# Kernel optimization log

Measured on AMD Instinct MI355X. Metric: run time of the kernel, lower is better.

Reference implementation:

```python
import jax, jax.numpy as jnp
import numpy as np

B, S, D, H = 4, 1024, 1024, 16
DK = D // H  # 64


def setup_inputs() -> dict:
    key = jax.random.key(0)
    ks = jax.random.split(key, 12)
    scale = 0.02
    inp = {
        "query": jax.random.normal(ks[0], (B, S, D), jnp.float32),
        "key": jax.random.normal(ks[1], (B, S, D), jnp.float32),
        "value": jax.random.normal(ks[2], (B, S, D), jnp.float32),
        "mask": jax.random.randint(ks[3], (B, 1, S, S), 0, 2, jnp.int32),
        "wq": jax.random.normal(ks[4], (D, D), jnp.float32) * scale,
        "bq": jnp.zeros((D,), jnp.float32),
        "wk": jax.random.normal(ks[5], (D, D), jnp.float32) * scale,
        "bk": jnp.zeros((D,), jnp.float32),
        "wv": jax.random.normal(ks[6], (D, D), jnp.float32) * scale,
        "bv": jnp.zeros((D,), jnp.float32),
        "wo": jax.random.normal(ks[7], (D, D), jnp.float32) * scale,
        "bo": jnp.zeros((D,), jnp.float32),
    }
    return inp


def reference(query, key, value, mask, wq, bq, wk, bk, wv, bv, wo, bo):
    # Linear projections (torch Linear: x @ W.T + b)
    q = query @ wq.T + bq
    k = key @ wk.T + bk
    v = value @ wv.T + bv
    # [B,S,D] -> [B,H,S,DK]
    q = q.reshape(B, S, H, DK).transpose(0, 2, 1, 3)
    k = k.reshape(B, S, H, DK).transpose(0, 2, 1, 3)
    v = v.reshape(B, S, H, DK).transpose(0, 2, 1, 3)
    # scaled dot-product attention with mask (-1e9 where mask==0)
    scores = jnp.einsum('bhqd,bhkd->bhqk', q, k) / jnp.sqrt(jnp.float32(DK))
    scores = jnp.where(mask == 0, jnp.float32(-1e9), scores)
    attn = jax.nn.softmax(scores, axis=-1)  # dropout p=0.0 -> identity
    x = jnp.einsum('bhqk,bhkd->bhqd', attn, v)
    # [B,H,S,DK] -> [B,S,D]
    x = x.transpose(0, 2, 1, 3).reshape(B, S, D)
    return x @ wo.T + bo
```

## Files before the change

kernel.cpp:

```cpp
#include <hip/hip_runtime.h>


typedef __attribute__((ext_vector_type(8))) short short8;
typedef __attribute__((ext_vector_type(4))) float f32x4;
typedef __attribute__((ext_vector_type(4))) unsigned short u16x4;
typedef unsigned short u16;
typedef unsigned long long u64;

#define SCALE_Q 0.180336880f

__device__ __forceinline__ u16 f2bf(float f) {
    unsigned u = __float_as_uint(f);
    return (u16)((u + 0x7FFFu + ((u >> 16) & 1u)) >> 16);
}
__device__ __forceinline__ u16 f2bf_fast(float f) {
    return (u16)((__float_as_uint(f) + 0x8000u) >> 16);
}
__device__ __forceinline__ float bf2f(u16 v) {
    return __uint_as_float((unsigned)v << 16);
}

__device__ __forceinline__ void gl_lds16(const u16* g, u16* l) {
    __builtin_amdgcn_global_load_lds(
        (__attribute__((address_space(1))) void*)g,
        (__attribute__((address_space(3))) void*)l, 16, 0, 0);
}

__global__ __launch_bounds__(256) void prep(
    const float* __restrict__ q, const float* __restrict__ k,
    const float* __restrict__ v, const float* __restrict__ wq,
    const float* __restrict__ wk, const float* __restrict__ wv,
    const float* __restrict__ wo, const int* __restrict__ mask,
    u16* __restrict__ xq, u16* __restrict__ xk, u16* __restrict__ xv,
    u16* __restrict__ wqb, u16* __restrict__ wkb, u16* __restrict__ wvb,
    u16* __restrict__ wob, u64* __restrict__ bits) {
    int bid = blockIdx.x;
    if (bid < 16384) {
        const float* src; u16* dst; int i;
        if (bid < 12288) {
            int chunk = bid >> 12;
            int off = bid & 4095;
            src = (chunk == 0) ? q : ((chunk == 1) ? k : v);
            dst = (chunk == 0) ? xq : ((chunk == 1) ? xk : xv);
            i = off * 256 + threadIdx.x;
        } else {
            int wb = bid - 12288;
            int chunk = wb >> 10;
            int off = wb & 1023;
            src = (chunk == 0) ? wq : ((chunk == 1) ? wk : ((chunk == 2) ? wv : wo));
            dst = (chunk == 0) ? wqb : ((chunk == 1) ? wkb : ((chunk == 2) ? wvb : wob));
            i = off * 256 + threadIdx.x;
        }
        f32x4 val = ((const f32x4*)src)[i];
        u16x4 r;
        r.x = f2bf(val.x); r.y = f2bf(val.y); r.z = f2bf(val.z); r.w = f2bf(val.w);
        ((u16x4*)dst)[i] = r;
    } else {
        int mb = bid - 16384;
        int wid = threadIdx.x >> 6, lane = threadIdx.x & 63;
        int base = mb * 1024 + wid * 256;
        int b = mb >> 10, qrow = mb & 1023;
        #pragma unroll
        for (int j = 0; j < 4; ++j) {
            u64 bal = __ballot(mask[base + j * 64 + lane] != 0);
            int kt = wid * 4 + j;
            if (lane == 0) bits[(size_t)(b * 16 + kt) * 1024 + qrow] = bal;
        }
    }
}

__global__ __launch_bounds__(256, 3) void gemm_qkv(
    const u16* __restrict__ Aq, const u16* __restrict__ Ak, const u16* __restrict__ Av,
    const u16* __restrict__ Wq, const u16* __restrict__ Wk, const u16* __restrict__ Wv,
    const float* __restrict__ bq, const float* __restrict__ bk, const float* __restrict__ bv,
    u16* __restrict__ Qo, u16* __restrict__ Ko, u16* __restrict__ VTo) {
    __shared__ __align__(16) u16 As[128 * 64];
    __shared__ __align__(16) u16 Bs[128 * 64];
    const int id = blockIdx.x;
    const int n0 = (id / 96) * 128;
    const int pm = id % 96;
    const int p = pm >> 5;
    const int m0 = (pm & 31) * 128;
    const u16* A = (p == 0) ? Aq : ((p == 1) ? Ak : Av);
    const u16* W = (p == 0) ? Wq : ((p == 1) ? Wk : Wv);
    const float* bias = (p == 0) ? bq : ((p == 1) ? bk : bv);

    const int t = threadIdx.x;
    const int lane = t & 63;
    const int wid = t >> 6;
    const int l15 = lane & 15;
    const int quad = lane >> 4;
    const int wm = (wid & 1) * 64;
    const int wn = (wid >> 1) * 64;
    const int r8 = lane >> 3, gr = lane & 7;
    const int gsw = (gr ^ r8) * 8;

    f32x4 acc[4][4];
    #pragma unroll
    for (int i = 0; i < 4; ++i)
        #pragma unroll
        for (int j = 0; j < 4; ++j) acc[i][j] = (f32x4){0.f, 0.f, 0.f, 0.f};

    for (int kt = 0; kt < 1024; kt += 64) {
        __syncthreads();
        #pragma unroll
        for (int c = 0; c < 8; ++c) {
            int call = wid * 8 + c;
            if (call < 16) {
                int rb = call * 8;
                gl_lds16(&A[(size_t)(m0 + rb + r8) * 1024 + kt + gsw], &As[rb * 64]);
            } else {
                int rb = (call - 16) * 8;
                gl_lds16(&W[(size_t)(n0 + rb + r8) * 1024 + kt + gsw], &Bs[rb * 64]);
            }
        }
        __syncthreads();
        #pragma unroll
        for (int ks = 0; ks < 2; ++ks) {
            short8 af[4], bf[4];
            #pragma unroll
            for (int i = 0; i < 4; ++i) {
                int mr = wm + i * 16 + l15;
                af[i] = *(const short8*)&As[mr * 64 + (((ks << 2) + quad) ^ (mr & 7)) * 8];
                int nr = wn + i * 16 + l15;
                bf[i] = *(const short8*)&Bs[nr * 64 + (((ks << 2) + quad) ^ (nr & 7)) * 8];
            }
            #pragma unroll
            for (int mi = 0; mi < 4; ++mi)
                #pragma unroll
                for (int ni = 0; ni < 4; ++ni)
                    acc[mi][ni] = __builtin_amdgcn_mfma_f32_16x16x32_bf16(
                        af[mi], bf[ni], acc[mi][ni], 0, 0, 0);
        }
    }

    u16* dst01 = (p == 0) ? Qo : Ko;
    const float qs = (p == 0) ? SCALE_Q : 1.0f;
    #pragma unroll
    for (int mi = 0; mi < 4; ++mi) {
        #pragma unroll
        for (int ni = 0; ni < 4; ++ni) {
            int col = n0 + wn + ni * 16 + l15;
            int h = col >> 6, dk = col & 63;
            float bcol = bias[col];
            if (p < 2) {
                #pragma unroll
                for (int r = 0; r < 4; ++r) {
                    int row = m0 + wm + mi * 16 + quad * 4 + r;
                    int bb = row >> 10, s = row & 1023;
                    dst01[(size_t)((bb * 16 + h) * 1024 + s) * 64 + dk] =
                        f2bf((acc[mi][ni][r] + bcol) * qs);
                }
            } else {
                int row0 = m0 + wm + mi * 16 + quad * 4;
                int bb = row0 >> 10, s0 = row0 & 1023;
                u64 pk = 0;
                #pragma unroll
                for (int r = 0; r < 4; ++r)
                    pk |= (u64)f2bf(acc[mi][ni][r] + bcol) << (16 * r);
                *(u64*)&VTo[(size_t)((bb * 16 + h) * 64 + dk) * 1024 + s0] = pk;
            }
        }
    }
}

__global__ __launch_bounds__(256, 3) void gemm_out(
    const u16* __restrict__ X, const u16* __restrict__ Wo,
    const float* __restrict__ bo, float* __restrict__ out) {
    __shared__ __align__(16) u16 As[64 * 64];
    __shared__ __align__(16) u16 Bs[128 * 64];
    const int id = blockIdx.x;
    const int n0 = (id >> 6) * 128;
    const int m0 = (id & 63) * 64;
    const int t = threadIdx.x;
    const int lane = t & 63;
    const int wid = t >> 6;
    const int l15 = lane & 15;
    const int quad = lane >> 4;
    const int wm = (wid & 1) * 32;
    const int wn = (wid >> 1) * 64;
    const int r8 = lane >> 3, gr = lane & 7;
    const int gsw = (gr ^ r8) * 8;

    f32x4 acc[2][4];
    #pragma unroll
    for (int i = 0; i < 2; ++i)
        #pragma unroll
        for (int j = 0; j < 4; ++j) acc[i][j] = (f32x4){0.f, 0.f, 0.f, 0.f};

    for (int kt = 0; kt < 1024; kt += 64) {
        __syncthreads();
        #pragma unroll
        for (int c = 0; c < 6; ++c) {
            int call = wid * 6 + c;
            if (call < 8) {
                int rb = call * 8;
                gl_lds16(&X[(size_t)(m0 + rb + r8) * 1024 + kt + gsw], &As[rb * 64]);
            } else {
                int rb = (call - 8) * 8;
                gl_lds16(&Wo[(size_t)(n0 + rb + r8) * 1024 + kt + gsw], &Bs[rb * 64]);
            }
        }
        __syncthreads();
        #pragma unroll
        for (int ks = 0; ks < 2; ++ks) {
            short8 af[2], bf[4];
            #pragma unroll
            for (int i = 0; i < 2; ++i) {
                int mr = wm + i * 16 + l15;
                af[i] = *(const short8*)&As[mr * 64 + (((ks << 2) + quad) ^ (mr & 7)) * 8];
            }
            #pragma unroll
            for (int j = 0; j < 4; ++j) {
                int nr = wn + j * 16 + l15;
                bf[j] = *(const short8*)&Bs[nr * 64 + (((ks << 2) + quad) ^ (nr & 7)) * 8];
            }
            #pragma unroll
            for (int mi = 0; mi < 2; ++mi)
                #pragma unroll
                for (int ni = 0; ni < 4; ++ni)
                    acc[mi][ni] = __builtin_amdgcn_mfma_f32_16x16x32_bf16(
                        af[mi], bf[ni], acc[mi][ni], 0, 0, 0);
        }
    }

    #pragma unroll
    for (int mi = 0; mi < 2; ++mi) {
        #pragma unroll
        for (int ni = 0; ni < 4; ++ni) {
            int col = n0 + wn + ni * 16 + l15;
            float bcol = bo[col];
            #pragma unroll
            for (int r = 0; r < 4; ++r) {
                int row = m0 + wm + mi * 16 + quad * 4 + r;
                out[(size_t)row * 1024 + col] = acc[mi][ni][r] + bcol;
            }
        }
    }
}

__global__ __launch_bounds__(256) void attn_kernel(
    const u16* __restrict__ Q, const u16* __restrict__ K, const u16* __restrict__ VT,
    const u64* __restrict__ mbits, u16* __restrict__ O, float* __restrict__ L) {
    __shared__ __align__(16) u16 Ks[64 * 64];
    __shared__ __align__(16) u16 Vs[64 * 64];
    __shared__ __align__(16) u16 Ps[4][16 * 72];

    const int qt = blockIdx.x;
    const int h = blockIdx.y;
    const int b = blockIdx.z >> 1;
    const int half = blockIdx.z & 1;
    const int t = threadIdx.x;
    const int lane = t & 63;
    const int wid = t >> 6;
    const int l15 = lane & 15;
    const int quad = lane >> 4;
    const int q0 = qt * 64;
    const int sr = t >> 3;
    const int sc = t & 7;
    const int ktg0 = half * 8;

    const size_t headoff = (size_t)(b * 16 + h) * 1024 * 64;
    const u16* Qh = Q + headoff;
    const u16* Kh = K + headoff;
    const u16* Vh = VT + headoff;

    short8 qf[2];
    #pragma unroll
    for (int ks = 0; ks < 2; ++ks)
        qf[ks] = *(const short8*)&Qh[(size_t)(q0 + wid * 16 + l15) * 64 + ks * 32 + quad * 8];

    f32x4 o_acc[4];
    #pragma unroll
    for (int j = 0; j < 4; ++j) o_acc[j] = (f32x4){0.f, 0.f, 0.f, 0.f};
    float lacc = 0.f;

    const u64* mbase = &mbits[(size_t)(b * 16) * 1024 + q0 + wid * 16 + l15];

    short8 kpre[2], vpre[2];
    #pragma unroll
    for (int p = 0; p < 2; ++p) {
        int r = p * 32 + sr;
        kpre[p] = *(const short8*)&Kh[(size_t)(ktg0 * 64 + r) * 64 + sc * 8];
        vpre[p] = *(const short8*)&Vh[(size_t)r * 1024 + ktg0 * 64 + sc * 8];
    }

    for (int kt = 0; kt < 8; ++kt) {
        __syncthreads();
        #pragma unroll
        for (int p = 0; p < 2; ++p) {
            int r = p * 32 + sr;
            int gl = sc ^ (r & 7);
            *(short8*)&Ks[r * 64 + gl * 8] = kpre[p];
            *(short8*)&Vs[r * 64 + gl * 8] = vpre[p];
        }
        __syncthreads();

        if (kt < 7) {
            int kvn = (ktg0 + kt + 1) * 64;
            #pragma unroll
            for (int p = 0; p < 2; ++p) {
                int r = p * 32 + sr;
                kpre[p] = *(const short8*)&Kh[(size_t)(kvn + r) * 64 + sc * 8];
                vpre[p] = *(const short8*)&Vh[(size_t)r * 1024 + kvn + sc * 8];
            }
        }

        f32x4 sacc[4];
        #pragma unroll
        for (int j = 0; j < 4; ++j) sacc[j] = (f32x4){0.f, 0.f, 0.f, 0.f};
        #pragma unroll
        for (int ks = 0; ks < 2; ++ks) {
            #pragma unroll
            for (int mi = 0; mi < 4; ++mi) {
                int n = mi * 16 + l15;
                short8 kf = *(const short8*)&Ks[n * 64 + (((ks << 2) + quad) ^ (n & 7)) * 8];
                sacc[mi] = __builtin_amdgcn_mfma_f32_16x16x32_bf16(kf, qf[ks], sacc[mi], 0, 0, 0);
            }
        }

        u64 w = mbase[(size_t)(ktg0 + kt) * 1024];
        unsigned t0 = (unsigned)(w >> (quad * 4));
        unsigned t1 = (unsigned)(w >> (quad * 4 + 32));
        #pragma unroll
        for (int mi = 0; mi < 4; ++mi) {
            unsigned sel = (mi & 2) ? t1 : t0;
            sel >>= (mi & 1) * 16;
            u64 pk = 0;
            #pragma unroll
            for (int r = 0; r < 4; ++r) {
                float p = __builtin_amdgcn_exp2f(sacc[mi][r]);
                p = ((sel >> r) & 1u) ? p : 0.f;
                lacc += p;
                pk |= (u64)f2bf_fast(p) << (16 * r);
            }
            *(u64*)&Ps[wid][l15 * 72 + mi * 16 + quad * 4] = pk;
        }

        #pragma unroll
        for (int ks = 0; ks < 2; ++ks) {
            short8 pf = *(const short8*)&Ps[wid][l15 * 72 + ks * 32 + quad * 8];
            #pragma unroll
            for (int j = 0; j < 4; ++j) {
                int d = j * 16 + l15;
                short8 vf = *(const short8*)&Vs[d * 64 + (((ks << 2) + quad) ^ (d & 7)) * 8];
                o_acc[j] = __builtin_amdgcn_mfma_f32_16x16x32_bf16(pf, vf, o_acc[j], 0, 0, 0);
            }
        }
    }

    float l = lacc;
    l += __shfl_xor(l, 16);
    l += __shfl_xor(l, 32);
    u16* Oh = O + (size_t)half * 4194304;
    float* Lh = L + (size_t)half * 65536;
    if (lane < 16)
        Lh[(size_t)(b * 16 + h) * 1024 + q0 + wid * 16 + lane] = l;
    #pragma unroll
    for (int r = 0; r < 4; ++r) {
        int qrow = q0 + wid * 16 + quad * 4 + r;
        #pragma unroll
        for (int ni = 0; ni < 4; ++ni) {
            Oh[(size_t)(b * 1024 + qrow) * 1024 + h * 64 + ni * 16 + l15] =
                f2bf(o_acc[ni][r]);
        }
    }
}

__global__ __launch_bounds__(256) void merge_halves(
    const u16* __restrict__ O, const float* __restrict__ L, u16* __restrict__ X) {
    int i = (blockIdx.x * 256 + threadIdx.x) * 8;
    int b = i >> 20, s = (i >> 10) & 1023, c = i & 1023, h = c >> 6;
    short8 o0 = *(const short8*)&O[i];
    short8 o1 = *(const short8*)&O[4194304 + i];
    size_t li = (size_t)(b * 16 + h) * 1024 + s;
    float inv = 1.0f / (L[li] + L[65536 + li]);
    short8 r;
    #pragma unroll
    for (int j = 0; j < 8; ++j) {
        float x = (bf2f((u16)o0[j]) + bf2f((u16)o1[j])) * inv;
        r[j] = (short)f2bf(x);
    }
    *(short8*)&X[i] = r;
}

extern "C" void kernel_launch(void* const* d_in, const int* in_sizes, int n_in,
                              void* d_out, int out_size, void* d_ws, size_t ws_size,
                              hipStream_t stream) {
    const float* query = (const float*)d_in[0];
    const float* key_ = (const float*)d_in[1];
    const float* value = (const float*)d_in[2];
    const int* mask = (const int*)d_in[3];
    const float* wq = (const float*)d_in[4];
    const float* bq = (const float*)d_in[5];
    const float* wk = (const float*)d_in[6];
    const float* bk = (const float*)d_in[7];
    const float* wv = (const float*)d_in[8];
    const float* bv = (const float*)d_in[9];
    const float* wo = (const float*)d_in[10];
    const float* bo = (const float*)d_in[11];
    float* out = (float*)d_out;

    char* ws = (char*)d_ws;
    const size_t XB = (size_t)4096 * 1024 * 2;
    const size_t WB = (size_t)1024 * 1024 * 2;
    u16* xq = (u16*)(ws);
    u16* xk = (u16*)(ws + XB);
    u16* xv = (u16*)(ws + 2 * XB);
    u16* wqb = (u16*)(ws + 3 * XB);
    u16* wkb = (u16*)(ws + 3 * XB + WB);
    u16* wvb = (u16*)(ws + 3 * XB + 2 * WB);
    u16* wob = (u16*)(ws + 3 * XB + 3 * WB);
    u16* Qb = (u16*)(ws + 3 * XB + 4 * WB);
    u16* Kb = (u16*)(ws + 4 * XB + 4 * WB);
    u16* VTb = (u16*)(ws + 5 * XB + 4 * WB);
    u64* bits = (u64*)(ws + 6 * XB + 4 * WB);
    float* Lbuf = (float*)(ws + 6 * XB + 4 * WB + (512 << 10));
    u16* Opart = xk;
    u16* Xattn = xq;

    prep<<<20480, 256, 0, stream>>>(query, key_, value, wq, wk, wv, wo, mask,
                                    xq, xk, xv, wqb, wkb, wvb, wob, bits);
    gemm_qkv<<<768, 256, 0, stream>>>(xq, xk, xv, wqb, wkb, wvb,
                                      bq, bk, bv, Qb, Kb, VTb);
    attn_kernel<<<dim3(16, 16, 8), 256, 0, stream>>>(Qb, Kb, VTb, bits, Opart, Lbuf);
    merge_halves<<<2048, 256, 0, stream>>>(Opart, Lbuf, Xattn);
    gemm_out<<<512, 256, 0, stream>>>(Xattn, wob, bo, out);
}
```

Baseline: 222.2 us.

## Fuse split-KV merge into output GEMM and double query rows per attention block

Removes the merge_halves kernel by performing the two-half normalization and bf16 conversion inside gemm_out's A-tile load, writing the merged tile into LDS directly instead of via async global-to-LDS copies. The attention kernel now processes 32 query rows per wave (128 per block), reusing each K/V LDS tile across twice as many queries and halving the grid. This cuts a kernel launch and a full intermediate write/read, but the merge math is recomputed by each of the 8 N-column blocks sharing an M tile. The attention kernel also uses more registers per thread.

```diff
diff --git a/kernel.cpp b/kernel.cpp
--- a/kernel.cpp
+++ b/kernel.cpp
@@ -165,8 +165,9 @@
 }
 
 __global__ __launch_bounds__(256, 3) void gemm_out(
-    const u16* __restrict__ X, const u16* __restrict__ Wo,
-    const float* __restrict__ bo, float* __restrict__ out) {
+    const u16* __restrict__ O, const float* __restrict__ L,
+    const u16* __restrict__ Wo, const float* __restrict__ bo,
+    float* __restrict__ out) {
     __shared__ __align__(16) u16 As[64 * 64];
     __shared__ __align__(16) u16 Bs[128 * 64];
     const int id = blockIdx.x;
@@ -181,6 +182,7 @@
     const int wn = (wid >> 1) * 64;
     const int r8 = lane >> 3, gr = lane & 7;
     const int gsw = (gr ^ r8) * 8;
+    const int sr = t >> 3, sc = t & 7;
 
     f32x4 acc[2][4];
     #pragma unroll
@@ -189,17 +191,28 @@
         for (int j = 0; j < 4; ++j) acc[i][j] = (f32x4){0.f, 0.f, 0.f, 0.f};
 
     for (int kt = 0; kt < 1024; kt += 64) {
-        __syncthreads();
-        #pragma unroll
-        for (int c = 0; c < 6; ++c) {
-            int call = wid * 6 + c;
-            if (call < 8) {
-                int rb = call * 8;
-                gl_lds16(&X[(size_t)(m0 + rb + r8) * 1024 + kt + gsw], &As[rb * 64]);
-            } else {
-                int rb = (call - 8) * 8;
-                gl_lds16(&Wo[(size_t)(n0 + rb + r8) * 1024 + kt + gsw], &Bs[rb * 64]);
-            }
+        const int h = kt >> 6;
+        __syncthreads();
+        #pragma unroll
+        for (int p = 0; p < 2; ++p) {
+            int r = p * 32 + sr;
+            int row = m0 + r;
+            int b = row >> 10, s = row & 1023;
+            size_t li = (size_t)((b * 16 + h) << 10) + s;
+            float inv = 1.0f / (L[li] + L[65536 + li]);
+            size_t go = (size_t)row * 1024 + kt + sc * 8;
+            short8 o0 = *(const short8*)&O[go];
+            short8 o1 = *(const short8*)&O[4194304 + go];
+            short8 xm;
+            #pragma unroll
+            for (int j = 0; j < 8; ++j)
+                xm[j] = (short)f2bf((bf2f((u16)o0[j]) + bf2f((u16)o1[j])) * inv);
+            *(short8*)&As[r * 64 + (sc ^ (r & 7)) * 8] = xm;
+        }
+        #pragma unroll
+        for (int c = 0; c < 4; ++c) {
+            int rb = (wid * 4 + c) * 8;
+            gl_lds16(&Wo[(size_t)(n0 + rb + r8) * 1024 + kt + gsw], &Bs[rb * 64]);
         }
         __syncthreads();
         #pragma unroll
@@ -239,12 +252,12 @@
     }
 }
 
-__global__ __launch_bounds__(256) void attn_kernel(
+__global__ __launch_bounds__(256, 4) void attn_kernel(
     const u16* __restrict__ Q, const u16* __restrict__ K, const u16* __restrict__ VT,
     const u64* __restrict__ mbits, u16* __restrict__ O, float* __restrict__ L) {
     __shared__ __align__(16) u16 Ks[64 * 64];
     __shared__ __align__(16) u16 Vs[64 * 64];
-    __shared__ __align__(16) u16 Ps[4][16 * 72];
+    __shared__ __align__(16) u16 Ps[4][32 * 72];
 
     const int qt = blockIdx.x;
     const int h = blockIdx.y;
@@ -255,7 +268,7 @@
     const int wid = t >> 6;
     const int l15 = lane & 15;
     const int quad = lane >> 4;
-    const int q0 = qt * 64;
+    const int q0 = qt * 128;
     const int sr = t >> 3;
     const int sc = t & 7;
     const int ktg0 = half * 8;
@@ -265,17 +278,22 @@
     const u16* Kh = K + headoff;
     const u16* Vh = VT + headoff;
 
-    short8 qf[2];
-    #pragma unroll
-    for (int ks = 0; ks < 2; ++ks)
-        qf[ks] = *(const short8*)&Qh[(size_t)(q0 + wid * 16 + l15) * 64 + ks * 32 + quad * 8];
-
-    f32x4 o_acc[4];
-    #pragma unroll
-    for (int j = 0; j < 4; ++j) o_acc[j] = (f32x4){0.f, 0.f, 0.f, 0.f};
-    float lacc = 0.f;
-
-    const u64* mbase = &mbits[(size_t)(b * 16) * 1024 + q0 + wid * 16 + l15];
+    short8 qf[2][2];
+    #pragma unroll
+    for (int qi = 0; qi < 2; ++qi)
+        #pragma unroll
+        for (int ks = 0; ks < 2; ++ks)
+            qf[qi][ks] = *(const short8*)&Qh[(size_t)(q0 + wid * 32 + qi * 16 + l15) * 64
+                                             + ks * 32 + quad * 8];
+
+    f32x4 o_acc[2][4];
+    #pragma unroll
+    for (int qi = 0; qi < 2; ++qi)
+        #pragma unroll
+        for (int j = 0; j < 4; ++j) o_acc[qi][j] = (f32x4){0.f, 0.f, 0.f, 0.f};
+    float lacc[2] = {0.f, 0.f};
+
+    const u64* mrow = &mbits[(size_t)(b * 16) * 1024 + q0 + wid * 32 + l15];
 
     short8 kpre[2], vpre[2];
     #pragma unroll
@@ -306,82 +324,73 @@
             }
         }
 
-        f32x4 sacc[4];
-        #pragma unroll
-        for (int j = 0; j < 4; ++j) sacc[j] = (f32x4){0.f, 0.f, 0.f, 0.f};
-        #pragma unroll
-        for (int ks = 0; ks < 2; ++ks) {
+        #pragma unroll
+        for (int qi = 0; qi < 2; ++qi) {
+            f32x4 sacc[4];
+            #pragma unroll
+            for (int j = 0; j < 4; ++j) sacc[j] = (f32x4){0.f, 0.f, 0.f, 0.f};
+            #pragma unroll
+            for (int ks = 0; ks < 2; ++ks) {
+                #pragma unroll
+                for (int mi = 0; mi < 4; ++mi) {
+                    int n = mi * 16 + l15;
+                    short8 kf = *(const short8*)&Ks[n * 64 + (((ks << 2) + quad) ^ (n & 7)) * 8];
+                    sacc[mi] = __builtin_amdgcn_mfma_f32_16x16x32_bf16(
+                        kf, qf[qi][ks], sacc[mi], 0, 0, 0);
+                }
+            }
+
+            u64 w = mrow[(size_t)(ktg0 + kt) * 1024 + qi * 16];
+            unsigned t0 = (unsigned)(w >> (quad * 4));
+            unsigned t1 = (unsigned)(w >> (quad * 4 + 32));
             #pragma unroll
             for (int mi = 0; mi < 4; ++mi) {
-                int n = mi * 16 + l15;
-                short8 kf = *(const short8*)&Ks[n * 64 + (((ks << 2) + quad) ^ (n & 7)) * 8];
-                sacc[mi] = __builtin_amdgcn_mfma_f32_16x16x32_bf16(kf, qf[ks], sacc[mi], 0, 0, 0);
-            }
-        }
-
-        u64 w = mbase[(size_t)(ktg0 + kt) * 1024];
-        unsigned t0 = (unsigned)(w >> (quad * 4));
-        unsigned t1 = (unsigned)(w >> (quad * 4 + 32));
-        #pragma unroll
-        for (int mi = 0; mi < 4; ++mi) {
-            unsigned sel = (mi & 2) ? t1 : t0;
-            sel >>= (mi & 1) * 16;
-            u64 pk = 0;
-            #pragma unroll
-            for (int r = 0; r < 4; ++r) {
-                float p = __builtin_amdgcn_exp2f(sacc[mi][r]);
-                p = ((sel >> r) & 1u) ? p : 0.f;
-                lacc += p;
-                pk |= (u64)f2bf_fast(p) << (16 * r);
-            }
-            *(u64*)&Ps[wid][l15 * 72 + mi * 16 + quad * 4] = pk;
-        }
-
-        #pragma unroll
-        for (int ks = 0; ks < 2; ++ks) {
-            short8 pf = *(const short8*)&Ps[wid][l15 * 72 + ks * 32 + quad * 8];
-            #pragma unroll
-            for (int j = 0; j < 4; ++j) {
-                int d = j * 16 + l15;
-                short8 vf = *(const short8*)&Vs[d * 64 + (((ks << 2) + quad) ^ (d & 7)) * 8];
-                o_acc[j] = __builtin_amdgcn_mfma_f32_16x16x32_bf16(pf, vf, o_acc[j], 0, 0, 0);
-            }
-        }
-    }
-
-    float l = lacc;
-    l += __shfl_xor(l, 16);
-    l += __shfl_xor(l, 32);
+                unsigned sel = (mi & 2) ? t1 : t0;
+                sel >>= (mi & 1) * 16;
+                u64 pk = 0;
+                #pragma unroll
+                for (int r = 0; r < 4; ++r) {
+                    float p = __builtin_amdgcn_exp2f(sacc[mi][r]);
+                    p = ((sel >> r) & 1u) ? p : 0.f;
+                    lacc[qi] += p;
+                    pk |= (u64)f2bf_fast(p) << (16 * r);
+                }
+                *(u64*)&Ps[wid][(qi * 16 + l15) * 72 + mi * 16 + quad * 4] = pk;
+            }
+
+            #pragma unroll
+            for (int ks = 0; ks < 2; ++ks) {
+                short8 pf = *(const short8*)&Ps[wid][(qi * 16 + l15) * 72 + ks * 32 + quad * 8];
+                #pragma unroll
+                for (int j = 0; j < 4; ++j) {
+                    int d = j * 16 + l15;
+                    short8 vf = *(const short8*)&Vs[d * 64 + (((ks << 2) + quad) ^ (d & 7)) * 8];
+                    o_acc[qi][j] = __builtin_amdgcn_mfma_f32_16x16x32_bf16(
+                        pf, vf, o_acc[qi][j], 0, 0, 0);
+                }
+            }
+        }
+    }
+
     u16* Oh = O + (size_t)half * 4194304;
     float* Lh = L + (size_t)half * 65536;
-    if (lane < 16)
-        Lh[(size_t)(b * 16 + h) * 1024 + q0 + wid * 16 + lane] = l;
-    #pragma unroll
-    for (int r = 0; r < 4; ++r) {
-        int qrow = q0 + wid * 16 + quad * 4 + r;
-        #pragma unroll
-        for (int ni = 0; ni < 4; ++ni) {
-            Oh[(size_t)(b * 1024 + qrow) * 1024 + h * 64 + ni * 16 + l15] =
-                f2bf(o_acc[ni][r]);
-        }
-    }
-}
-
-__global__ __launch_bounds__(256) void merge_halves(
-    const u16* __restrict__ O, const float* __restrict__ L, u16* __restrict__ X) {
-    int i = (blockIdx.x * 256 + threadIdx.x) * 8;
-    int b = i >> 20, s = (i >> 10) & 1023, c = i & 1023, h = c >> 6;
-    short8 o0 = *(const short8*)&O[i];
-    short8 o1 = *(const short8*)&O[4194304 + i];
-    size_t li = (size_t)(b * 16 + h) * 1024 + s;
-    float inv = 1.0f / (L[li] + L[65536 + li]);
-    short8 r;
-    #pragma unroll
-    for (int j = 0; j < 8; ++j) {
-        float x = (bf2f((u16)o0[j]) + bf2f((u16)o1[j])) * inv;
-        r[j] = (short)f2bf(x);
-    }
-    *(short8*)&X[i] = r;
+    #pragma unroll
+    for (int qi = 0; qi < 2; ++qi) {
+        float l = lacc[qi];
+        l += __shfl_xor(l, 16);
+        l += __shfl_xor(l, 32);
+        if (lane < 16)
+            Lh[(size_t)(b * 16 + h) * 1024 + q0 + wid * 32 + qi * 16 + lane] = l;
+        #pragma unroll
+        for (int r = 0; r < 4; ++r) {
+            int qrow = q0 + wid * 32 + qi * 16 + quad * 4 + r;
+            #pragma unroll
+            for (int ni = 0; ni < 4; ++ni) {
+                Oh[(size_t)(b * 1024 + qrow) * 1024 + h * 64 + ni * 16 + l15] =
+                    f2bf(o_acc[qi][ni][r]);
+            }
+        }
+    }
 }
 
 extern "C" void kernel_launch(void* const* d_in, const int* in_sizes, int n_in,
@@ -417,13 +426,11 @@
     u64* bits = (u64*)(ws + 6 * XB + 4 * WB);
     float* Lbuf = (float*)(ws + 6 * XB + 4 * WB + (512 << 10));
     u16* Opart = xk;
-    u16* Xattn = xq;
 
     prep<<<20480, 256, 0, stream>>>(query, key_, value, wq, wk, wv, wo, mask,
                                     xq, xk, xv, wqb, wkb, wvb, wob, bits);
     gemm_qkv<<<768, 256, 0, stream>>>(xq, xk, xv, wqb, wkb, wvb,
                                       bq, bk, bv, Qb, Kb, VTb);
-    attn_kernel<<<dim3(16, 16, 8), 256, 0, stream>>>(Qb, Kb, VTb, bits, Opart, Lbuf);
-    merge_halves<<<2048, 256, 0, stream>>>(Opart, Lbuf, Xattn);
-    gemm_out<<<512, 256, 0, stream>>>(Xattn, wob, bo, out);
-}
+    attn_kernel<<<dim3(8, 16, 8), 256, 0, stream>>>(Qb, Kb, VTb, bits, Opart, Lbuf);
+    gemm_out<<<512, 256, 0, stream>>>(Opart, Lbuf, wob, bo, out);
+}
```

Result: slower. 236.6 us (+6.5%).

## Load K/V fragments directly from global memory, dropping LDS staging and barriers

Applied to the files above, without the earlier changes.

The attention kernel stops staging K and V tiles through shared memory with register prefetch and two block barriers per tile. Each wave now loads its MFMA operand fragments for K and V^T straight from global memory into registers. This removes the LDS traffic and the __syncthreads calls. The cost is that all four waves load the same K/V data redundantly through L1/L2, and the cross-iteration prefetch that hid global latency is gone.

```diff
diff --git a/kernel.cpp b/kernel.cpp
--- a/kernel.cpp
+++ b/kernel.cpp
@@ -242,8 +242,6 @@
 __global__ __launch_bounds__(256) void attn_kernel(
     const u16* __restrict__ Q, const u16* __restrict__ K, const u16* __restrict__ VT,
     const u64* __restrict__ mbits, u16* __restrict__ O, float* __restrict__ L) {
-    __shared__ __align__(16) u16 Ks[64 * 64];
-    __shared__ __align__(16) u16 Vs[64 * 64];
     __shared__ __align__(16) u16 Ps[4][16 * 72];
 
     const int qt = blockIdx.x;
@@ -256,8 +254,6 @@
     const int l15 = lane & 15;
     const int quad = lane >> 4;
     const int q0 = qt * 64;
-    const int sr = t >> 3;
-    const int sc = t & 7;
     const int ktg0 = half * 8;
 
     const size_t headoff = (size_t)(b * 16 + h) * 1024 * 64;
@@ -277,47 +273,33 @@
 
     const u64* mbase = &mbits[(size_t)(b * 16) * 1024 + q0 + wid * 16 + l15];
 
-    short8 kpre[2], vpre[2];
-    #pragma unroll
-    for (int p = 0; p < 2; ++p) {
-        int r = p * 32 + sr;
-        kpre[p] = *(const short8*)&Kh[(size_t)(ktg0 * 64 + r) * 64 + sc * 8];
-        vpre[p] = *(const short8*)&Vh[(size_t)r * 1024 + ktg0 * 64 + sc * 8];
-    }
-
     for (int kt = 0; kt < 8; ++kt) {
-        __syncthreads();
-        #pragma unroll
-        for (int p = 0; p < 2; ++p) {
-            int r = p * 32 + sr;
-            int gl = sc ^ (r & 7);
-            *(short8*)&Ks[r * 64 + gl * 8] = kpre[p];
-            *(short8*)&Vs[r * 64 + gl * 8] = vpre[p];
-        }
-        __syncthreads();
-
-        if (kt < 7) {
-            int kvn = (ktg0 + kt + 1) * 64;
-            #pragma unroll
-            for (int p = 0; p < 2; ++p) {
-                int r = p * 32 + sr;
-                kpre[p] = *(const short8*)&Kh[(size_t)(kvn + r) * 64 + sc * 8];
-                vpre[p] = *(const short8*)&Vh[(size_t)r * 1024 + kvn + sc * 8];
-            }
-        }
+        const int kv0 = (ktg0 + kt) * 64;
+
+        short8 kf[2][4];
+        #pragma unroll
+        for (int ks = 0; ks < 2; ++ks)
+            #pragma unroll
+            for (int mi = 0; mi < 4; ++mi)
+                kf[ks][mi] = *(const short8*)&Kh[(size_t)(kv0 + mi * 16 + l15) * 64
+                                                 + ks * 32 + quad * 8];
+        short8 vf[2][4];
+        #pragma unroll
+        for (int ks = 0; ks < 2; ++ks)
+            #pragma unroll
+            for (int j = 0; j < 4; ++j)
+                vf[ks][j] = *(const short8*)&Vh[(size_t)(j * 16 + l15) * 1024
+                                                + kv0 + ks * 32 + quad * 8];
 
         f32x4 sacc[4];
         #pragma unroll
         for (int j = 0; j < 4; ++j) sacc[j] = (f32x4){0.f, 0.f, 0.f, 0.f};
         #pragma unroll
-        for (int ks = 0; ks < 2; ++ks) {
-            #pragma unroll
-            for (int mi = 0; mi < 4; ++mi) {
-                int n = mi * 16 + l15;
-                short8 kf = *(const short8*)&Ks[n * 64 + (((ks << 2) + quad) ^ (n & 7)) * 8];
-                sacc[mi] = __builtin_amdgcn_mfma_f32_16x16x32_bf16(kf, qf[ks], sacc[mi], 0, 0, 0);
-            }
-        }
+        for (int ks = 0; ks < 2; ++ks)
+            #pragma unroll
+            for (int mi = 0; mi < 4; ++mi)
+                sacc[mi] = __builtin_amdgcn_mfma_f32_16x16x32_bf16(
+                    kf[ks][mi], qf[ks], sacc[mi], 0, 0, 0);
 
         u64 w = mbase[(size_t)(ktg0 + kt) * 1024];
         unsigned t0 = (unsigned)(w >> (quad * 4));
@@ -341,11 +323,9 @@
         for (int ks = 0; ks < 2; ++ks) {
             short8 pf = *(const short8*)&Ps[wid][l15 * 72 + ks * 32 + quad * 8];
             #pragma unroll
-            for (int j = 0; j < 4; ++j) {
-                int d = j * 16 + l15;
-                short8 vf = *(const short8*)&Vs[d * 64 + (((ks << 2) + quad) ^ (d & 7)) * 8];
-                o_acc[j] = __builtin_amdgcn_mfma_f32_16x16x32_bf16(pf, vf, o_acc[j], 0, 0, 0);
-            }
+            for (int j = 0; j < 4; ++j)
+                o_acc[j] = __builtin_amdgcn_mfma_f32_16x16x32_bf16(
+                    pf, vf[ks][j], o_acc[j], 0, 0, 0);
         }
     }
 
```

New measurement: 312.5 us. 1.41x slower.
